# Kernel optimization log

Hardware: AMD Instinct MI355X
Metric: run time of the kernel (lower is better)

Reference implementation:

```python
import jax, jax.numpy as jnp
import numpy as np

B, D_IN, H, K = 16384, 256, 1024, 16


def setup_inputs() -> dict:
    key = jax.random.key(0)
    k_x, k_idx, k_w1, k_w2 = jax.random.split(key, 4)
    x = jax.random.normal(k_x, (B, D_IN), dtype=jnp.float32)
    input_indices = jax.random.randint(k_idx, (H, K), 0, D_IN, dtype=jnp.int64)
    w1 = jax.random.normal(k_w1, (H, K), dtype=jnp.float32) * np.sqrt(2.0 / K).astype(np.float32)
    b1 = jnp.zeros((H,), dtype=jnp.float32)
    w2 = jax.random.normal(k_w2, (1, H), dtype=jnp.float32) * np.sqrt(2.0 / H).astype(np.float32)
    b2 = jnp.zeros((1,), dtype=jnp.float32)
    return {"x": x, "input_indices": input_indices, "w1": w1, "b1": b1, "w2": w2, "b2": b2}


def reference(x, input_indices, w1, b1, w2, b2):
    # Gather per-neuron inputs: [B, H, K] (vectorized form of the torch per-h loop)
    selected = x[:, input_indices]
    # Per-neuron weighted sum + bias, tanh
    pre_act = jnp.einsum('bhk,hk->bh', selected, w1) + b1  # [B, H]
    hidden = jnp.tanh(pre_act)
    # Output linear + tanh, squeeze to [B]
    out = jnp.tanh(hidden @ w2.T + b2)  # [B, 1]
    return out.squeeze(-1)
```

## Files before the change

kernel.cpp:

```cpp
#include <hip/hip_runtime.h>
#include <hip/hip_fp16.h>

#define NB 16384
#define ND 256
#define NH 1024
#define NK 16

using f16x8 = __attribute__((ext_vector_type(8))) _Float16;
using f32x4 = __attribute__((ext_vector_type(4))) float;

__device__ __forceinline__ float fast_tanh(float x) {
    float e = __expf(2.0f * x);
    return 1.0f - 2.0f * __builtin_amdgcn_rcpf(e + 1.0f);
}

__device__ __forceinline__ void scat8(float (&a)[8], int ii, float ww, int d0) {
#pragma unroll
    for (int e = 0; e < 8; ++e)
        if (ii == d0 + e) a[e] += ww;
}

__global__ __launch_bounds__(128) void build_w_kernel(
        const int* __restrict__ idx, const float* __restrict__ w1,
        _Float16* __restrict__ Wf) {
    int t = blockIdx.x * 128 + threadIdx.x;
    int h = t >> 5;
    int g = t & 31;
    int d0 = g << 3;
    const int4*   ip = reinterpret_cast<const int4*>(idx + h * NK);
    const float4* wp = reinterpret_cast<const float4*>(w1 + h * NK);
    float a[8];
#pragma unroll
    for (int e = 0; e < 8; ++e) a[e] = 0.f;
#pragma unroll
    for (int j = 0; j < 4; ++j) {
        int4   I = ip[j];
        float4 V = wp[j];
        scat8(a, I.x, V.x, d0);
        scat8(a, I.y, V.y, d0);
        scat8(a, I.z, V.z, d0);
        scat8(a, I.w, V.w, d0);
    }
    int c  = h >> 4;
    int ml = h & 15;
    int ks = g >> 2;
    int kg = g & 3;
    size_t off = (((size_t)(c * 8 + ks)) * 64 + kg * 16 + ml) * 8;
    f16x8 o;
#pragma unroll
    for (int e = 0; e < 8; ++e) o[e] = (_Float16)a[e];
    *reinterpret_cast<f16x8*>(&Wf[off]) = o;
}

__global__ __launch_bounds__(512, 2) void fused_kernel(
        const float* __restrict__ x, const _Float16* __restrict__ Wf,
        const float* __restrict__ b1, const float* __restrict__ w2,
        const float* __restrict__ b2, float* __restrict__ out) {
    __shared__ _Float16 lA[64 * 256];
    __shared__ float red[8 * 64];

    const int t = threadIdx.x;
    const int lane = t & 63;
    const int w = t >> 6;
    const int gm0 = blockIdx.x * 64;
    const int ml = lane & 15;
    const int kg = lane >> 4;
    const int start = ((blockIdx.x >> 3) + w) & 7;

    const int sr  = t >> 3;
    const int sub = t & 7;
    const float4* xsrc = reinterpret_cast<const float4*>(
        x + (size_t)(gm0 + sr) * ND + sub * 32);
    float4 v[8];
#pragma unroll
    for (int j = 0; j < 8; ++j) v[j] = xsrc[j];

    const _Float16* gW = Wf + (size_t)w * 32768 + (size_t)lane * 8;
    f16x8 bA[4], bB[4];
    {
        const _Float16* p0 = gW + start * 4096;
#pragma unroll
        for (int ks = 0; ks < 4; ++ks)
            bA[ks] = *reinterpret_cast<const f16x8*>(p0 + ks * 512);
#pragma unroll
        for (int ks = 0; ks < 4; ++ks)
            bB[ks] = *reinterpret_cast<const f16x8*>(p0 + 2048 + ks * 512);
    }

#pragma unroll
    for (int q = 0; q < 4; ++q) {
        int c = sub * 4 + q;
        f16x8 hh;
        hh[0] = (_Float16)v[2*q].x;   hh[1] = (_Float16)v[2*q].y;
        hh[2] = (_Float16)v[2*q].z;   hh[3] = (_Float16)v[2*q].w;
        hh[4] = (_Float16)v[2*q+1].x; hh[5] = (_Float16)v[2*q+1].y;
        hh[6] = (_Float16)v[2*q+1].z; hh[7] = (_Float16)v[2*q+1].w;
        int a16 = sr * 32 + (c ^ (sr & 7));
        *reinterpret_cast<f16x8*>(&lA[a16 * 8]) = hh;
    }
    __syncthreads();

    f16x8 af[4][8];
#pragma unroll
    for (int mi = 0; mi < 4; ++mi)
#pragma unroll
        for (int ks = 0; ks < 8; ++ks) {
            int r = mi * 16 + ml;
            int c = ks * 4 + kg;
            af[mi][ks] = *reinterpret_cast<const f16x8*>(
                &lA[(r * 32 + (c ^ (r & 7))) * 8]);
        }

    float rowpart[4][4];
#pragma unroll
    for (int mi = 0; mi < 4; ++mi)
#pragma unroll
        for (int r4 = 0; r4 < 4; ++r4) rowpart[mi][r4] = 0.f;

#pragma unroll 1
    for (int nc = 0; nc < 8; ++nc) {
        const int ncc = (start + nc) & 7;
        float b1v = b1[w * 128 + ncc * 16 + ml];
        float w2v = w2[w * 128 + ncc * 16 + ml];

        f32x4 acc[4];
#pragma unroll
        for (int mi = 0; mi < 4; ++mi) acc[mi] = f32x4{0.f, 0.f, 0.f, 0.f};

        const int ncn = (start + nc + 1) & 7;
        const _Float16* pn = gW + ncn * 4096;

        __builtin_amdgcn_s_setprio(1);
#pragma unroll
        for (int ks = 0; ks < 4; ++ks)
#pragma unroll
            for (int mi = 0; mi < 4; ++mi)
                acc[mi] = __builtin_amdgcn_mfma_f32_16x16x32_f16(
                    af[mi][ks], bA[ks], acc[mi], 0, 0, 0);
        __builtin_amdgcn_s_setprio(0);
        if (nc != 7) {
#pragma unroll
            for (int ks = 0; ks < 4; ++ks)
                bA[ks] = *reinterpret_cast<const f16x8*>(pn + ks * 512);
        }

        __builtin_amdgcn_s_setprio(1);
#pragma unroll
        for (int ks = 0; ks < 4; ++ks)
#pragma unroll
            for (int mi = 0; mi < 4; ++mi)
                acc[mi] = __builtin_amdgcn_mfma_f32_16x16x32_f16(
                    af[mi][4 + ks], bB[ks], acc[mi], 0, 0, 0);
        __builtin_amdgcn_s_setprio(0);
        if (nc != 7) {
#pragma unroll
            for (int ks = 0; ks < 4; ++ks)
                bB[ks] = *reinterpret_cast<const f16x8*>(pn + 2048 + ks * 512);
        }

#pragma unroll
        for (int mi = 0; mi < 4; ++mi)
#pragma unroll
            for (int r4 = 0; r4 < 4; ++r4)
                rowpart[mi][r4] += fast_tanh(acc[mi][r4] + b1v) * w2v;
    }

#pragma unroll
    for (int mi = 0; mi < 4; ++mi)
#pragma unroll
        for (int r4 = 0; r4 < 4; ++r4) {
            float vv = rowpart[mi][r4];
            vv += __shfl_xor(vv, 1);
            vv += __shfl_xor(vv, 2);
            vv += __shfl_xor(vv, 4);
            vv += __shfl_xor(vv, 8);
            rowpart[mi][r4] = vv;
        }
    if (ml == 0) {
#pragma unroll
        for (int mi = 0; mi < 4; ++mi)
#pragma unroll
            for (int r4 = 0; r4 < 4; ++r4)
                red[w * 64 + mi * 16 + kg * 4 + r4] = rowpart[mi][r4];
    }
    __syncthreads();

    if (t < 64) {
        float s = 0.f;
#pragma unroll
        for (int j = 0; j < 8; ++j) s += red[j * 64 + t];
        out[gm0 + t] = fast_tanh(s + b2[0]);
    }
}

extern "C" void kernel_launch(void* const* d_in, const int* in_sizes, int n_in,
                              void* d_out, int out_size, void* d_ws, size_t ws_size,
                              hipStream_t stream) {
    const float* x   = (const float*)d_in[0];
    const int*   idx = (const int*)d_in[1];
    const float* w1  = (const float*)d_in[2];
    const float* b1  = (const float*)d_in[3];
    const float* w2  = (const float*)d_in[4];
    const float* b2  = (const float*)d_in[5];
    float* out = (float*)d_out;

    _Float16* Wf = (_Float16*)d_ws;

    build_w_kernel<<<(NH * 32) / 128, 128, 0, stream>>>(idx, w1, Wf);
    fused_kernel<<<NB / 64, 512, 0, stream>>>(x, Wf, b1, w2, b2, out);
}
```

Baseline: 22.46 us.

## Split hidden dimension across two blocks with 2x4 wave tiling and final reduce kernel

The fused kernel now launches a 2D grid in which each block covers half the hidden units, and waves are arranged as 2 row-groups by 4 column-groups, so each wave holds half as many A fragments. Per-block partial sums go to workspace and a new small kernel adds the two halves, applies b2 and the output tanh. Launch bounds are raised to allow 4 blocks per SM, and tanh is rewritten with exp2 and FMA folding of the bias. The intent is more parallelism and occupancy. The cost is reloading and converting x into LDS twice, an extra launch, and a partial-buffer round trip.

```diff
diff --git a/kernel.cpp b/kernel.cpp
--- a/kernel.cpp
+++ b/kernel.cpp
@@ -9,10 +9,7 @@
 using f16x8 = __attribute__((ext_vector_type(8))) _Float16;
 using f32x4 = __attribute__((ext_vector_type(4))) float;
 
-__device__ __forceinline__ float fast_tanh(float x) {
-    float e = __expf(2.0f * x);
-    return 1.0f - 2.0f * __builtin_amdgcn_rcpf(e + 1.0f);
-}
+#define C2LOG2E 2.8853900817779268f
 
 __device__ __forceinline__ void scat8(float (&a)[8], int ii, float ww, int d0) {
 #pragma unroll
@@ -52,20 +49,24 @@
     *reinterpret_cast<f16x8*>(&Wf[off]) = o;
 }
 
-__global__ __launch_bounds__(512, 2) void fused_kernel(
+__global__ __launch_bounds__(512, 4) void fused_kernel(
         const float* __restrict__ x, const _Float16* __restrict__ Wf,
         const float* __restrict__ b1, const float* __restrict__ w2,
-        const float* __restrict__ b2, float* __restrict__ out) {
+        float* __restrict__ partial) {
     __shared__ _Float16 lA[64 * 256];
-    __shared__ float red[8 * 64];
+    __shared__ float red[4 * 64];
 
     const int t = threadIdx.x;
     const int lane = t & 63;
     const int w = t >> 6;
-    const int gm0 = blockIdx.x * 64;
+    const int r = w >> 2;
+    const int c = w & 3;
+    const int bx = blockIdx.x;
+    const int by = blockIdx.y;
+    const int gm0 = bx * 64;
     const int ml = lane & 15;
     const int kg = lane >> 4;
-    const int start = ((blockIdx.x >> 3) + w) & 7;
+    const int start = (bx + c) & 7;
 
     const int sr  = t >> 3;
     const int sub = t & 7;
@@ -75,66 +76,68 @@
 #pragma unroll
     for (int j = 0; j < 8; ++j) v[j] = xsrc[j];
 
-    const _Float16* gW = Wf + (size_t)w * 32768 + (size_t)lane * 8;
-    f16x8 bA[4], bB[4];
-    {
-        const _Float16* p0 = gW + start * 4096;
-#pragma unroll
-        for (int ks = 0; ks < 4; ++ks)
-            bA[ks] = *reinterpret_cast<const f16x8*>(p0 + ks * 512);
-#pragma unroll
-        for (int ks = 0; ks < 4; ++ks)
-            bB[ks] = *reinterpret_cast<const f16x8*>(p0 + 2048 + ks * 512);
-    }
-
 #pragma unroll
     for (int q = 0; q < 4; ++q) {
-        int c = sub * 4 + q;
+        int cc = sub * 4 + q;
         f16x8 hh;
         hh[0] = (_Float16)v[2*q].x;   hh[1] = (_Float16)v[2*q].y;
         hh[2] = (_Float16)v[2*q].z;   hh[3] = (_Float16)v[2*q].w;
         hh[4] = (_Float16)v[2*q+1].x; hh[5] = (_Float16)v[2*q+1].y;
         hh[6] = (_Float16)v[2*q+1].z; hh[7] = (_Float16)v[2*q+1].w;
-        int a16 = sr * 32 + (c ^ (sr & 7));
+        int a16 = sr * 32 + (cc ^ (sr & 7));
         *reinterpret_cast<f16x8*>(&lA[a16 * 8]) = hh;
     }
     __syncthreads();
 
-    f16x8 af[4][8];
-#pragma unroll
-    for (int mi = 0; mi < 4; ++mi)
+    f16x8 af[2][8];
+#pragma unroll
+    for (int mi = 0; mi < 2; ++mi)
 #pragma unroll
         for (int ks = 0; ks < 8; ++ks) {
-            int r = mi * 16 + ml;
-            int c = ks * 4 + kg;
+            int row = r * 32 + mi * 16 + ml;
+            int cc  = ks * 4 + kg;
             af[mi][ks] = *reinterpret_cast<const f16x8*>(
-                &lA[(r * 32 + (c ^ (r & 7))) * 8]);
-        }
-
-    float rowpart[4][4];
-#pragma unroll
-    for (int mi = 0; mi < 4; ++mi)
+                &lA[(row * 32 + (cc ^ (row & 7))) * 8]);
+        }
+
+    const int cbase = by * 32 + c * 8;
+    const _Float16* gW = Wf + (size_t)cbase * 4096 + (size_t)lane * 8;
+    f16x8 bA[4], bB[4];
+    {
+        const _Float16* p0 = gW + start * 4096;
+#pragma unroll
+        for (int ks = 0; ks < 4; ++ks)
+            bA[ks] = *reinterpret_cast<const f16x8*>(p0 + ks * 512);
+#pragma unroll
+        for (int ks = 0; ks < 4; ++ks)
+            bB[ks] = *reinterpret_cast<const f16x8*>(p0 + 2048 + ks * 512);
+    }
+
+    float rowpart[2][4];
+#pragma unroll
+    for (int mi = 0; mi < 2; ++mi)
 #pragma unroll
         for (int r4 = 0; r4 < 4; ++r4) rowpart[mi][r4] = 0.f;
+
+    const int colbase = (cbase << 4) + ml;
 
 #pragma unroll 1
     for (int nc = 0; nc < 8; ++nc) {
         const int ncc = (start + nc) & 7;
-        float b1v = b1[w * 128 + ncc * 16 + ml];
-        float w2v = w2[w * 128 + ncc * 16 + ml];
-
-        f32x4 acc[4];
-#pragma unroll
-        for (int mi = 0; mi < 4; ++mi) acc[mi] = f32x4{0.f, 0.f, 0.f, 0.f};
-
-        const int ncn = (start + nc + 1) & 7;
-        const _Float16* pn = gW + ncn * 4096;
+        float b1v = b1[colbase + ncc * 16];
+        float w2v = w2[colbase + ncc * 16];
+
+        f32x4 acc[2];
+#pragma unroll
+        for (int mi = 0; mi < 2; ++mi) acc[mi] = f32x4{0.f, 0.f, 0.f, 0.f};
+
+        const _Float16* pn = gW + (((start + nc + 1) & 7) * 4096);
 
         __builtin_amdgcn_s_setprio(1);
 #pragma unroll
         for (int ks = 0; ks < 4; ++ks)
 #pragma unroll
-            for (int mi = 0; mi < 4; ++mi)
+            for (int mi = 0; mi < 2; ++mi)
                 acc[mi] = __builtin_amdgcn_mfma_f32_16x16x32_f16(
                     af[mi][ks], bA[ks], acc[mi], 0, 0, 0);
         __builtin_amdgcn_s_setprio(0);
@@ -148,7 +151,7 @@
 #pragma unroll
         for (int ks = 0; ks < 4; ++ks)
 #pragma unroll
-            for (int mi = 0; mi < 4; ++mi)
+            for (int mi = 0; mi < 2; ++mi)
                 acc[mi] = __builtin_amdgcn_mfma_f32_16x16x32_f16(
                     af[mi][4 + ks], bB[ks], acc[mi], 0, 0, 0);
         __builtin_amdgcn_s_setprio(0);
@@ -158,15 +161,21 @@
                 bB[ks] = *reinterpret_cast<const f16x8*>(pn + 2048 + ks * 512);
         }
 
-#pragma unroll
-        for (int mi = 0; mi < 4; ++mi)
-#pragma unroll
-            for (int r4 = 0; r4 < 4; ++r4)
-                rowpart[mi][r4] += fast_tanh(acc[mi][r4] + b1v) * w2v;
-    }
-
-#pragma unroll
-    for (int mi = 0; mi < 4; ++mi)
+        float b1c = b1v * C2LOG2E;
+#pragma unroll
+        for (int mi = 0; mi < 2; ++mi)
+#pragma unroll
+            for (int r4 = 0; r4 < 4; ++r4) {
+                float arg = __builtin_fmaf(acc[mi][r4], C2LOG2E, b1c);
+                float e = __builtin_exp2f(arg);
+                float rc = __builtin_amdgcn_rcpf(e + 1.0f);
+                float th = __builtin_fmaf(-2.f, rc, 1.f);
+                rowpart[mi][r4] = __builtin_fmaf(th, w2v, rowpart[mi][r4]);
+            }
+    }
+
+#pragma unroll
+    for (int mi = 0; mi < 2; ++mi)
 #pragma unroll
         for (int r4 = 0; r4 < 4; ++r4) {
             float vv = rowpart[mi][r4];
@@ -178,19 +187,27 @@
         }
     if (ml == 0) {
 #pragma unroll
-        for (int mi = 0; mi < 4; ++mi)
+        for (int mi = 0; mi < 2; ++mi)
 #pragma unroll
             for (int r4 = 0; r4 < 4; ++r4)
-                red[w * 64 + mi * 16 + kg * 4 + r4] = rowpart[mi][r4];
+                red[c * 64 + r * 32 + mi * 16 + kg * 4 + r4] = rowpart[mi][r4];
     }
     __syncthreads();
 
     if (t < 64) {
-        float s = 0.f;
-#pragma unroll
-        for (int j = 0; j < 8; ++j) s += red[j * 64 + t];
-        out[gm0 + t] = fast_tanh(s + b2[0]);
-    }
+        float s = red[t] + red[64 + t] + red[128 + t] + red[192 + t];
+        partial[(size_t)by * NB + gm0 + t] = s;
+    }
+}
+
+__global__ __launch_bounds__(256) void final_kernel(
+        const float* __restrict__ partial, const float* __restrict__ b2,
+        float* __restrict__ out) {
+    int i = blockIdx.x * 256 + threadIdx.x;
+    float s = partial[i] + partial[NB + i] + b2[0];
+    float arg = s * C2LOG2E;
+    float e = __builtin_exp2f(arg);
+    out[i] = 1.0f - 2.0f * __builtin_amdgcn_rcpf(e + 1.0f);
 }
 
 extern "C" void kernel_launch(void* const* d_in, const int* in_sizes, int n_in,
@@ -204,8 +221,10 @@
     const float* b2  = (const float*)d_in[5];
     float* out = (float*)d_out;
 
-    _Float16* Wf = (_Float16*)d_ws;
+    _Float16* Wf    = (_Float16*)d_ws;
+    float*    partial = (float*)((char*)d_ws + (1u << 20));
 
     build_w_kernel<<<(NH * 32) / 128, 128, 0, stream>>>(idx, w1, Wf);
-    fused_kernel<<<NB / 64, 512, 0, stream>>>(x, Wf, b1, w2, b2, out);
-}
+    fused_kernel<<<dim3(NB / 64, 2), 512, 0, stream>>>(x, Wf, b1, w2, partial);
+    final_kernel<<<NB / 256, 256, 0, stream>>>(partial, b2, out);
+}
```

Result: slower. 31.25 us (+39.1%).
